# Kernel tuning notes

Measured on AMD Instinct MI355X. Metric: run time of the kernel, lower is better.

Reference implementation:

```python
import jax, jax.numpy as jnp
import numpy as np

B, N, CIN, H, W = 4, 1024, 256, 256, 256
R, C = 32, 32            # N = R*C table grid cells
PH, PW, SR = 3, 3, 2     # pool_size, sampling_ratio
D = 512                  # out_channels
SCALE = 0.25             # spatial_scale: image coords -> feature coords
IMG = 1024.0             # image size (H/SCALE)


def setup_inputs() -> dict:
    key = jax.random.key(0)
    ks = jax.random.split(key, 12)
    feats = jax.random.normal(ks[0], (B, CIN, H, W), jnp.float32)
    # build valid quadrilateral boxes (axis-aligned rectangles as 8-pt polys)
    x1 = jax.random.uniform(ks[1], (B, N), minval=0.0, maxval=IMG - 130.0)
    y1 = jax.random.uniform(ks[2], (B, N), minval=0.0, maxval=IMG - 130.0)
    bw = jax.random.uniform(ks[3], (B, N), minval=16.0, maxval=128.0)
    bh = jax.random.uniform(ks[4], (B, N), minval=16.0, maxval=128.0)
    x2, y2 = x1 + bw, y1 + bh
    boxes = jnp.stack([x1, y1, x2, y1, x2, y2, x1, y2], axis=-1)  # [B,N,8]
    img_sizes = jnp.full((B, 2), IMG, jnp.float32)
    IN = CIN * PH * PW
    W1 = jax.random.normal(ks[5], (IN, D), jnp.float32) * 0.02
    b1 = jnp.zeros((D,), jnp.float32)
    W2 = jax.random.normal(ks[6], (D, D), jnp.float32) * 0.02
    b2 = jnp.zeros((D,), jnp.float32)
    Wb = jax.random.normal(ks[7], (4, D), jnp.float32) * 0.02
    bb = jnp.zeros((D,), jnp.float32)
    g1 = jnp.ones((D,), jnp.float32); be1 = jnp.zeros((D,), jnp.float32)
    g2 = jnp.ones((D,), jnp.float32); be2 = jnp.zeros((D,), jnp.float32)
    return {"feats": feats, "boxes": boxes, "img_sizes": img_sizes,
            "W1": W1, "b1": b1, "W2": W2, "b2": b2, "Wb": Wb, "bb": bb,
            "g1": g1, "be1": be1, "g2": g2, "be2": be2}


def _layer_norm(x, g, b, eps=1e-5):
    mu = jnp.mean(x, axis=-1, keepdims=True)
    var = jnp.mean(jnp.square(x - mu), axis=-1, keepdims=True)
    return (x - mu) * jax.lax.rsqrt(var + eps) * g + b


def _bilinear(img, ys, xs):
    # img [Cin,H,W]; ys,xs [P] -> [Cin,P]; torchvision roi_align semantics:
    # zero outside (-1, dim); clamp into [0, dim-1] before interpolation.
    h, w = img.shape[1], img.shape[2]
    valid = (ys > -1.0) & (ys < h) & (xs > -1.0) & (xs < w)
    y = jnp.clip(ys, 0.0, h - 1.0)
    x = jnp.clip(xs, 0.0, w - 1.0)
    y0 = jnp.floor(y).astype(jnp.int32); x0 = jnp.floor(x).astype(jnp.int32)
    y1 = jnp.minimum(y0 + 1, h - 1);     x1 = jnp.minimum(x0 + 1, w - 1)
    ly = y - y0; lx = x - x0; hy = 1.0 - ly; hx = 1.0 - lx
    v = (img[:, y0, x0] * (hy * hx) + img[:, y0, x1] * (hy * lx)
         + img[:, y1, x0] * (ly * hx) + img[:, y1, x1] * (ly * lx))
    return v * valid


def _roi_align_one(img, bb):
    # img [Cin,H,W]; bb [N,4] already in feature coords -> [N,Cin,PH,PW]
    x1, y1, x2, y2 = bb[:, 0], bb[:, 1], bb[:, 2], bb[:, 3]
    rw = jnp.maximum(x2 - x1, 1.0); rh = jnp.maximum(y2 - y1, 1.0)
    binw = rw / PW; binh = rh / PH
    off = (jnp.arange(SR, dtype=jnp.float32) + 0.5) / SR
    gy = (jnp.arange(PH, dtype=jnp.float32)[:, None] + off[None, :]).reshape(-1)  # [PH*SR]
    gx = (jnp.arange(PW, dtype=jnp.float32)[:, None] + off[None, :]).reshape(-1)  # [PW*SR]
    ys = y1[:, None] + gy[None, :] * binh[:, None]  # [N,PH*SR]
    xs = x1[:, None] + gx[None, :] * binw[:, None]  # [N,PW*SR]
    YY = jnp.broadcast_to(ys[:, :, None], (bb.shape[0], PH * SR, PW * SR)).reshape(-1)
    XX = jnp.broadcast_to(xs[:, None, :], (bb.shape[0], PH * SR, PW * SR)).reshape(-1)
    vals = _bilinear(img, YY, XX)  # [Cin, N*PH*SR*PW*SR]
    vals = vals.reshape(CIN, bb.shape[0], PH, SR, PW, SR).mean(axis=(3, 5))
    return vals.transpose(1, 0, 2, 3)


def reference(feats, boxes, img_sizes, W1, b1, W2, b2, Wb, bb, g1, be1, g2, be2):
    # poly2bbox: [B,N,8] -> [B,N,4] axis-aligned boxes
    px, py = boxes[..., 0::2], boxes[..., 1::2]
    bbox = jnp.stack([px.min(-1), py.min(-1), px.max(-1), py.max(-1)], axis=-1)
    # rotated/regular RoIAlign (here bbox path), vmapped over batch images
    pooled = jax.vmap(_roi_align_one)(feats, bbox * SCALE)     # [B,N,Cin,PH,PW]
    flat = pooled.reshape(B, N, CIN * PH * PW)
    lines_feat = jax.nn.relu(flat @ W1 + b1) @ W2 + b2          # [B,N,D]
    # bbox positional embedding (coords normalized by image size)
    denom = jnp.concatenate([img_sizes, img_sizes], axis=-1)[:, None, :]  # [B,1,4] (w,h,w,h)
    pos = _layer_norm(bbox / denom @ Wb + bb, g1, be1)
    out = _layer_norm(lines_feat + pos, g2, be2)                # [B,N,D]
    # align_cells_feat: pack cells into grid [B,D,R,C] (uniform grid -> no pad)
    aligned = out.transpose(0, 2, 1).reshape(B, D, R, C)
    masks = jnp.ones((B, R, C), jnp.float32)
    return aligned, masks
```

## Files before the change

### kernel.cpp

```cpp
#include <hip/hip_runtime.h>
#include <hip/hip_bf16.h>
#include <cstdint>
#include <cstddef>

#define B_    4
#define N_    1024
#define CIN_  256
#define HW_   256
#define D_    512
#define INK_  2304
#define BN_   4096

typedef __attribute__((ext_vector_type(8))) short bf16x8;
typedef __attribute__((ext_vector_type(4))) float f32x4;
typedef __attribute__((ext_vector_type(4))) unsigned short us4;

#define AS1(p) ((const __attribute__((address_space(1))) void*)(p))
#define AS3(p) ((__attribute__((address_space(3))) void*)(p))

__device__ __forceinline__ unsigned short f2bf(float f) {
    union { float f; unsigned u; } v; v.f = f;
    unsigned r = v.u + 0x7fffu + ((v.u >> 16) & 1u);
    return (unsigned short)(r >> 16);
}

template <typename OutT>
__global__ __launch_bounds__(256) void k_t64(
    const float* __restrict__ src, OutT* __restrict__ dst,
    int Mrows, int Ncols, size_t sBatch, size_t dBatch)
{
    constexpr int PAD = (sizeof(OutT) == 2) ? 66 : 67;
    __shared__ OutT tile[64][PAD];
    const int n0 = blockIdx.x * 64;
    const int m0 = blockIdx.y * 64;
    const float* s = src + (size_t)blockIdx.z * sBatch;
    OutT* d = dst + (size_t)blockIdx.z * dBatch;
    const int t  = threadIdx.x;
    const int rr = t >> 4;
    const int cc = t & 15;

    #pragma unroll
    for (int i = 0; i < 4; ++i) {
        int row = i * 16 + rr;
        float4 v = *(const float4*)(s + (size_t)(m0 + row) * Ncols + n0 + cc * 4);
        if constexpr (sizeof(OutT) == 2) {
            tile[row][cc * 4 + 0] = f2bf(v.x);
            tile[row][cc * 4 + 1] = f2bf(v.y);
            tile[row][cc * 4 + 2] = f2bf(v.z);
            tile[row][cc * 4 + 3] = f2bf(v.w);
        } else {
            tile[row][cc * 4 + 0] = v.x;
            tile[row][cc * 4 + 1] = v.y;
            tile[row][cc * 4 + 2] = v.z;
            tile[row][cc * 4 + 3] = v.w;
        }
    }
    __syncthreads();
    #pragma unroll
    for (int i = 0; i < 4; ++i) {
        int p = i * 16 + rr;
        OutT v0 = tile[cc * 4 + 0][p];
        OutT v1 = tile[cc * 4 + 1][p];
        OutT v2 = tile[cc * 4 + 2][p];
        OutT v3 = tile[cc * 4 + 3][p];
        OutT* dp = d + (size_t)(n0 + p) * Mrows + m0 + cc * 4;
        if constexpr (sizeof(OutT) == 2) {
            *(us4*)dp = (us4){(unsigned short)v0, (unsigned short)v1,
                              (unsigned short)v2, (unsigned short)v3};
        } else {
            *(float4*)dp = make_float4(v0, v1, v2, v3);
        }
    }
}

__global__ __launch_bounds__(256) void k_roi3(
    const unsigned short* __restrict__ featsT, const float* __restrict__ boxes,
    unsigned short* __restrict__ flat)
{
    __shared__ int   so[4][36][4];
    __shared__ float sw[4][36][4];
    const int t = threadIdx.x;

    if (t < 144) {
        const int mbx = t / 36, s = t - mbx * 36;
        const int mbn = blockIdx.x * 4 + mbx;
        const float* bx = boxes + (size_t)mbn * 8;
        float xmn = fminf(fminf(bx[0], bx[2]), fminf(bx[4], bx[6]));
        float xmx = fmaxf(fmaxf(bx[0], bx[2]), fmaxf(bx[4], bx[6]));
        float ymn = fminf(fminf(bx[1], bx[3]), fminf(bx[5], bx[7]));
        float ymx = fmaxf(fmaxf(bx[1], bx[3]), fmaxf(bx[5], bx[7]));
        float sx1 = xmn * 0.25f, sy1 = ymn * 0.25f;
        float sx2 = xmx * 0.25f, sy2 = ymx * 0.25f;
        float rw = fmaxf(sx2 - sx1, 1.0f), rh = fmaxf(sy2 - sy1, 1.0f);
        float binw = rw * (1.0f / 3.0f), binh = rh * (1.0f / 3.0f);
        int row = s / 6, col = s % 6;
        float y = sy1 + (row * 0.5f + 0.25f) * binh;
        float x = sx1 + (col * 0.5f + 0.25f) * binw;
        float valid = (y > -1.0f && y < 256.0f && x > -1.0f && x < 256.0f) ? 1.0f : 0.0f;
        y = fminf(fmaxf(y, 0.0f), 255.0f);
        x = fminf(fmaxf(x, 0.0f), 255.0f);
        int y0 = (int)floorf(y), x0 = (int)floorf(x);
        int y1 = min(y0 + 1, 255), x1 = min(x0 + 1, 255);
        float ly = y - (float)y0, lx = x - (float)x0;
        float hy = 1.0f - ly, hx = 1.0f - lx;
        float m = 0.25f * valid;
        so[mbx][s][0] = y0 * HW_ + x0;  so[mbx][s][1] = y0 * HW_ + x1;
        so[mbx][s][2] = y1 * HW_ + x0;  so[mbx][s][3] = y1 * HW_ + x1;
        sw[mbx][s][0] = hy * hx * m;    sw[mbx][s][1] = hy * lx * m;
        sw[mbx][s][2] = ly * hx * m;    sw[mbx][s][3] = ly * lx * m;
    }
    __syncthreads();

    const int bxi = t >> 6;
    const int tid = t & 63;
    const int bn  = blockIdx.x * 4 + bxi;
    const int b   = bn >> 10;
    const uint2* basep = (const uint2*)featsT + (size_t)b * (65536ull * 64ull) + tid;

    float a0[9] = {0,0,0,0,0,0,0,0,0};
    float a1[9] = {0,0,0,0,0,0,0,0,0};
    float a2[9] = {0,0,0,0,0,0,0,0,0};
    float a3[9] = {0,0,0,0,0,0,0,0,0};
    #pragma unroll
    for (int j = 0; j < 36; ++j) {
        const int bin = ((j / 6) >> 1) * 3 + ((j % 6) >> 1);
        #pragma unroll
        for (int p = 0; p < 4; ++p) {
            float wgt = sw[bxi][j][p];
            uint2 u = basep[(size_t)so[bxi][j][p] << 6];
            a0[bin] += wgt * __uint_as_float(u.x << 16);
            a1[bin] += wgt * __uint_as_float(u.x & 0xffff0000u);
            a2[bin] += wgt * __uint_as_float(u.y << 16);
            a3[bin] += wgt * __uint_as_float(u.y & 0xffff0000u);
        }
    }

    unsigned short tmp[36];
    #pragma unroll
    for (int k = 0; k < 9; ++k) {
        tmp[k] = f2bf(a0[k]); tmp[9 + k] = f2bf(a1[k]);
        tmp[18 + k] = f2bf(a2[k]); tmp[27 + k] = f2bf(a3[k]);
    }
    unsigned* dst = (unsigned*)(flat + (size_t)bn * INK_ + tid * 36);
    #pragma unroll
    for (int k = 0; k < 18; ++k)
        dst[k] = (unsigned)tmp[2 * k] | ((unsigned)tmp[2 * k + 1] << 16);
}

template <int K, bool RELU_BF16OUT>
__global__ __launch_bounds__(256) void k_gemmB(
    const unsigned short* __restrict__ A,
    const unsigned short* __restrict__ Bt,
    const float* __restrict__ bias,
    unsigned short* __restrict__ Cbf,
    float* __restrict__ Cf)
{
    __shared__ __align__(16) unsigned short As[2][128 * 32];
    __shared__ __align__(16) unsigned short Bs[2][64 * 32];

    const int t = threadIdx.x;
    const int w = t >> 6;
    const int lane = t & 63;
    const int lane16 = lane & 15;
    const int q = lane >> 4;
    const int m0 = blockIdx.x * 128;
    const int n0 = blockIdx.y * 64;

    const int r4 = lane >> 2, c4 = lane & 3;
    const int c4s = c4 ^ (r4 >> 2);
    const unsigned short* gA0 = A + (size_t)(m0 + w * 16 + r4) * K + c4s * 8;
    const unsigned short* gA1 = gA0 + (size_t)64 * K;
    const unsigned short* gB  = Bt + (size_t)(n0 + w * 16 + r4) * K + c4s * 8;

    const int qs = q ^ ((lane16 >> 2) & 3);

    f32x4 acc[2][4] = {};

    __builtin_amdgcn_global_load_lds(AS1(gA0), AS3(&As[0][(w * 16) * 32]), 16, 0, 0);
    __builtin_amdgcn_global_load_lds(AS1(gA1), AS3(&As[0][(64 + w * 16) * 32]), 16, 0, 0);
    __builtin_amdgcn_global_load_lds(AS1(gB ), AS3(&Bs[0][(w * 16) * 32]), 16, 0, 0);
    gA0 += 32; gA1 += 32; gB += 32;

    int cur = 0;
    for (int k0 = 0; k0 < K; k0 += 32) {
        __syncthreads();
        if (k0 + 32 < K) {
            __builtin_amdgcn_global_load_lds(AS1(gA0), AS3(&As[cur ^ 1][(w * 16) * 32]), 16, 0, 0);
            __builtin_amdgcn_global_load_lds(AS1(gA1), AS3(&As[cur ^ 1][(64 + w * 16) * 32]), 16, 0, 0);
            __builtin_amdgcn_global_load_lds(AS1(gB ), AS3(&Bs[cur ^ 1][(w * 16) * 32]), 16, 0, 0);
            gA0 += 32; gA1 += 32; gB += 32;
        }
        bf16x8 a0 = *(const bf16x8*)&As[cur][(w * 32 + lane16) * 32 + qs * 8];
        bf16x8 a1 = *(const bf16x8*)&As[cur][(w * 32 + 16 + lane16) * 32 + qs * 8];
        #pragma unroll
        for (int nt = 0; nt < 4; ++nt) {
            bf16x8 bv = *(const bf16x8*)&Bs[cur][(nt * 16 + lane16) * 32 + qs * 8];
            acc[0][nt] = __builtin_amdgcn_mfma_f32_16x16x32_bf16(a0, bv, acc[0][nt], 0, 0, 0);
            acc[1][nt] = __builtin_amdgcn_mfma_f32_16x16x32_bf16(a1, bv, acc[1][nt], 0, 0, 0);
        }
        cur ^= 1;
    }

    #pragma unroll
    for (int nt = 0; nt < 4; ++nt) {
        int col = n0 + nt * 16 + lane16;
        float bs = bias[col];
        #pragma unroll
        for (int mg = 0; mg < 2; ++mg) {
            #pragma unroll
            for (int r = 0; r < 4; ++r) {
                int row = m0 + w * 32 + mg * 16 + q * 4 + r;
                float v = acc[mg][nt][r] + bs;
                if constexpr (RELU_BF16OUT) {
                    v = fmaxf(v, 0.0f);
                    Cbf[(size_t)row * D_ + col] = f2bf(v);
                } else {
                    Cf[(size_t)row * D_ + col] = v;
                }
            }
        }
    }
}

__global__ __launch_bounds__(256) void k_fuse2(
    const unsigned short* __restrict__ act,
    const unsigned short* __restrict__ W2t,
    const float* __restrict__ b2,
    const float* __restrict__ boxes,
    const float* __restrict__ img_sizes,
    const float* __restrict__ Wb,  const float* __restrict__ bbv,
    const float* __restrict__ g1,  const float* __restrict__ be1,
    const float* __restrict__ g2,  const float* __restrict__ be2,
    float* __restrict__ out)
{
    __shared__ __align__(16) unsigned short Bs[2][512 * 32];
    float* S2 = (float*)&Bs[0][0];

    const int t = threadIdx.x;
    const int w = t >> 6, l = t & 63;
    const int lane16 = l & 15, q = l >> 4;
    const int m0 = blockIdx.x * 16;
    const int b  = m0 >> 10;

    const unsigned short* gB = W2t + (size_t)(t >> 2) * D_
                             + (size_t)(((t & 3) ^ ((t >> 4) & 3)) * 8);
    #pragma unroll
    for (int i = 0; i < 8; ++i)
        __builtin_amdgcn_global_load_lds(AS1(gB + (size_t)i * 64 * D_),
            AS3(&Bs[0][(t >> 2) * 32 + (t & 3) * 8 + i * 2048]), 16, 0, 0);

    const int qs = q ^ ((lane16 >> 2) & 3);

    f32x4 acc[8] = {};
    const unsigned short* gA = act + (size_t)(m0 + lane16) * D_ + q * 8;

    int cur = 0;
    for (int k0 = 0; k0 < D_; k0 += 32) {
        __syncthreads();
        bf16x8 av = *(const bf16x8*)(gA + k0);
        if (k0 + 32 < D_) {
            #pragma unroll
            for (int i = 0; i < 8; ++i)
                __builtin_amdgcn_global_load_lds(AS1(gB + k0 + 32 + (size_t)i * 64 * D_),
                    AS3(&Bs[cur ^ 1][(t >> 2) * 32 + (t & 3) * 8 + i * 2048]), 16, 0, 0);
        }
        #pragma unroll
        for (int nt = 0; nt < 8; ++nt) {
            bf16x8 bv = *(const bf16x8*)&Bs[cur][(w * 128 + nt * 16 + lane16) * 32 + qs * 8];
            acc[nt] = __builtin_amdgcn_mfma_f32_16x16x32_bf16(av, bv, acc[nt], 0, 0, 0);
        }
        cur ^= 1;
    }
    __syncthreads();

    #pragma unroll
    for (int nt = 0; nt < 8; ++nt) {
        int col = w * 128 + nt * 16 + lane16;
        float bs = b2[col];
        #pragma unroll
        for (int r = 0; r < 4; ++r)
            S2[(q * 4 + r) * D_ + col] = acc[nt][r] + bs;
    }
    __syncthreads();

    const float si0 = img_sizes[b * 2], si1 = img_sizes[b * 2 + 1];
    #pragma unroll 1
    for (int j = 0; j < 4; ++j) {
        const int rho = w * 4 + j;
        const float* bx = boxes + (size_t)(m0 + rho) * 8;
        float xmn = fminf(fminf(bx[0], bx[2]), fminf(bx[4], bx[6]));
        float xmx = fmaxf(fmaxf(bx[0], bx[2]), fmaxf(bx[4], bx[6]));
        float ymn = fminf(fminf(bx[1], bx[3]), fminf(bx[5], bx[7]));
        float ymx = fmaxf(fmaxf(bx[1], bx[3]), fmaxf(bx[5], bx[7]));
        float q0 = xmn / si0, q1 = ymn / si1, q2 = xmx / si0, q3 = ymx / si1;

        float tp[8], su = 0.f, sq = 0.f;
        #pragma unroll
        for (int i = 0; i < 8; ++i) {
            int d = i * 64 + l;
            float v = q0 * Wb[d] + q1 * Wb[512 + d] + q2 * Wb[1024 + d]
                    + q3 * Wb[1536 + d] + bbv[d];
            tp[i] = v; su += v; sq += v * v;
        }
        #pragma unroll
        for (int off = 32; off > 0; off >>= 1) {
            su += __shfl_xor(su, off); sq += __shfl_xor(sq, off);
        }
        float mu = su * (1.0f / 512.0f);
        float rs = rsqrtf(sq * (1.0f / 512.0f) - mu * mu + 1e-5f);

        float sv[8]; su = 0.f; sq = 0.f;
        #pragma unroll
        for (int i = 0; i < 8; ++i) {
            int d = i * 64 + l;
            float p = (tp[i] - mu) * rs * g1[d] + be1[d];
            float s = S2[rho * D_ + d] + p;
            sv[i] = s; su += s; sq += s * s;
        }
        #pragma unroll
        for (int off = 32; off > 0; off >>= 1) {
            su += __shfl_xor(su, off); sq += __shfl_xor(sq, off);
        }
        float mu2 = su * (1.0f / 512.0f);
        float rs2 = rsqrtf(sq * (1.0f / 512.0f) - mu2 * mu2 + 1e-5f);

        #pragma unroll
        for (int i = 0; i < 8; ++i) {
            int d = i * 64 + l;
            S2[rho * D_ + d] = (sv[i] - mu2) * rs2 * g2[d] + be2[d];
        }
    }
    __syncthreads();

    const int nb = m0 & 1023;
    float* ob = out + (size_t)b * (D_ * N_) + nb;
    const int dd = t >> 2, part = t & 3;
    #pragma unroll
    for (int i = 0; i < 8; ++i) {
        int d = i * 64 + dd;
        float4 v;
        v.x = S2[(part * 4 + 0) * D_ + d];
        v.y = S2[(part * 4 + 1) * D_ + d];
        v.z = S2[(part * 4 + 2) * D_ + d];
        v.w = S2[(part * 4 + 3) * D_ + d];
        *(float4*)(ob + (size_t)d * N_ + part * 4) = v;
    }
    if (t < 16) out[(size_t)B_ * D_ * N_ + m0 + t] = 1.0f;
}

__global__ __launch_bounds__(256) void k_convert(
    const float* __restrict__ W1, const float* __restrict__ W2,
    unsigned short* __restrict__ W1t, unsigned short* __restrict__ W2t)
{
    int i = blockIdx.x * 256 + threadIdx.x;
    const int n1 = INK_ * D_;
    if (i < n1) {
        int n = i / INK_, k = i % INK_;
        W1t[i] = f2bf(W1[(size_t)k * D_ + n]);
    } else {
        int j = i - n1;
        if (j < D_ * D_) {
            int n = j / D_, k = j % D_;
            W2t[j] = f2bf(W2[(size_t)k * D_ + n]);
        }
    }
}

__global__ __launch_bounds__(256) void k_roi(
    const float* __restrict__ feats, const float* __restrict__ boxes,
    unsigned short* __restrict__ flat)
{
    __shared__ int   so[36][4];
    __shared__ float sw[36][4];
    const int bn = blockIdx.x;
    const int b  = bn >> 10;
    const int t  = threadIdx.x;

    if (t < 36) {
        const float* bx = boxes + (size_t)bn * 8;
        float xmn = fminf(fminf(bx[0], bx[2]), fminf(bx[4], bx[6]));
        float xmx = fmaxf(fmaxf(bx[0], bx[2]), fmaxf(bx[4], bx[6]));
        float ymn = fminf(fminf(bx[1], bx[3]), fminf(bx[5], bx[7]));
        float ymx = fmaxf(fmaxf(bx[1], bx[3]), fmaxf(bx[5], bx[7]));
        float sx1 = xmn * 0.25f, sy1 = ymn * 0.25f;
        float sx2 = xmx * 0.25f, sy2 = ymx * 0.25f;
        float rw = fmaxf(sx2 - sx1, 1.0f), rh = fmaxf(sy2 - sy1, 1.0f);
        float binw = rw * (1.0f / 3.0f), binh = rh * (1.0f / 3.0f);
        int row = t / 6, col = t % 6;
        float y = sy1 + (row * 0.5f + 0.25f) * binh;
        float x = sx1 + (col * 0.5f + 0.25f) * binw;
        float valid = (y > -1.0f && y < 256.0f && x > -1.0f && x < 256.0f) ? 1.0f : 0.0f;
        y = fminf(fmaxf(y, 0.0f), 255.0f);
        x = fminf(fmaxf(x, 0.0f), 255.0f);
        int y0 = (int)floorf(y), x0 = (int)floorf(x);
        int y1 = min(y0 + 1, 255), x1 = min(x0 + 1, 255);
        float ly = y - (float)y0, lx = x - (float)x0;
        float hy = 1.0f - ly, hx = 1.0f - lx;
        float m = 0.25f * valid;
        so[t][0] = y0 * HW_ + x0;  so[t][1] = y0 * HW_ + x1;
        so[t][2] = y1 * HW_ + x0;  so[t][3] = y1 * HW_ + x1;
        sw[t][0] = hy * hx * m;    sw[t][1] = hy * lx * m;
        sw[t][2] = ly * hx * m;    sw[t][3] = ly * lx * m;
    }
    __syncthreads();

    const float* base = feats + ((size_t)(b * CIN_ + t) << 16);
    float acc[9] = {0.f,0.f,0.f,0.f,0.f,0.f,0.f,0.f,0.f};
    #pragma unroll
    for (int j = 0; j < 36; ++j) {
        const int bin = ((j / 6) >> 1) * 3 + ((j % 6) >> 1);
        float v = sw[j][0] * base[so[j][0]] + sw[j][1] * base[so[j][1]]
                + sw[j][2] * base[so[j][2]] + sw[j][3] * base[so[j][3]];
        acc[bin] += v;
    }
    unsigned short* dst = flat + (size_t)bn * INK_ + t * 9;
    #pragma unroll
    for (int k = 0; k < 9; ++k) dst[k] = f2bf(acc[k]);
}

template <int K, bool RELU_BF16OUT>
__global__ __launch_bounds__(256) void k_gemm(
    const unsigned short* __restrict__ A,
    const unsigned short* __restrict__ Bt,
    const float* __restrict__ bias,
    unsigned short* __restrict__ Cbf,
    float* __restrict__ Cf)
{
    __shared__ __align__(16) unsigned short Asl[64 * 40];
    __shared__ __align__(16) unsigned short Bsl[64 * 40];

    const int t  = threadIdx.x;
    const int m0 = blockIdx.x * 64;
    const int n0 = blockIdx.y * 64;
    const int w  = t >> 6;
    const int l  = t & 63;
    const int lane16 = l & 15;
    const int q  = l >> 4;

    f32x4 acc[4] = {};

    const int srow = t >> 2;
    const int sch  = t & 3;
    const unsigned short* ga = A  + (size_t)(m0 + srow) * K + sch * 8;
    const unsigned short* gb = Bt + (size_t)(n0 + srow) * K + sch * 8;
    unsigned short* la = &Asl[srow * 40 + sch * 8];
    unsigned short* lb = &Bsl[srow * 40 + sch * 8];

    for (int k0 = 0; k0 < K; k0 += 32) {
        __syncthreads();
        *(bf16x8*)la = *(const bf16x8*)(ga + k0);
        *(bf16x8*)lb = *(const bf16x8*)(gb + k0);
        __syncthreads();
        bf16x8 af = *(const bf16x8*)&Asl[(w * 16 + lane16) * 40 + q * 8];
        #pragma unroll
        for (int nt = 0; nt < 4; ++nt) {
            bf16x8 bfv = *(const bf16x8*)&Bsl[(nt * 16 + lane16) * 40 + q * 8];
            acc[nt] = __builtin_amdgcn_mfma_f32_16x16x32_bf16(af, bfv, acc[nt], 0, 0, 0);
        }
    }

    #pragma unroll
    for (int nt = 0; nt < 4; ++nt) {
        int col = n0 + nt * 16 + lane16;
        float bs = bias[col];
        #pragma unroll
        for (int r = 0; r < 4; ++r) {
            int rowg = m0 + w * 16 + q * 4 + r;
            float v = acc[nt][r] + bs;
            if constexpr (RELU_BF16OUT) {
                v = fmaxf(v, 0.0f);
                Cbf[(size_t)rowg * D_ + col] = f2bf(v);
            } else {
                Cf[(size_t)rowg * D_ + col] = v;
            }
        }
    }
}

__device__ __forceinline__ void breduce2(float& a, float& b, float* red, int t) {
    #pragma unroll
    for (int off = 32; off > 0; off >>= 1) {
        a += __shfl_down(a, off);
        b += __shfl_down(b, off);
    }
    int w = t >> 6;
    if ((t & 63) == 0) { red[w] = a; red[4 + w] = b; }
    __syncthreads();
    a = red[0] + red[1] + red[2] + red[3];
    b = red[4] + red[5] + red[6] + red[7];
    __syncthreads();
}

__global__ __launch_bounds__(256) void k_tail(
    const float* __restrict__ lines, const float* __restrict__ boxes,
    const float* __restrict__ img_sizes,
    const float* __restrict__ Wb,  const float* __restrict__ bbv,
    const float* __restrict__ g1,  const float* __restrict__ be1,
    const float* __restrict__ g2,  const float* __restrict__ be2,
    float* __restrict__ out)
{
    __shared__ float red[8];
    const int row = blockIdx.x;
    const int b = row >> 10, n = row & 1023;
    const int t = threadIdx.x;

    const float* bx = boxes + (size_t)row * 8;
    float xmn = fminf(fminf(bx[0], bx[2]), fminf(bx[4], bx[6]));
    float xmx = fmaxf(fmaxf(bx[0], bx[2]), fmaxf(bx[4], bx[6]));
    float ymn = fminf(fminf(bx[1], bx[3]), fminf(bx[5], bx[7]));
    float ymx = fmaxf(fmaxf(bx[1], bx[3]), fmaxf(bx[5], bx[7]));
    float s0 = img_sizes[b * 2], s1 = img_sizes[b * 2 + 1];
    float q0 = xmn / s0, q1 = ymn / s1, q2 = xmx / s0, q3 = ymx / s1;

    float tv[2], sv[2];
    float sum = 0.f, sumsq = 0.f;
    #pragma unroll
    for (int i = 0; i < 2; ++i) {
        int d = t + i * 256;
        float v = q0 * Wb[d] + q1 * Wb[512 + d] + q2 * Wb[1024 + d] + q3 * Wb[1536 + d] + bbv[d];
        tv[i] = v; sum += v; sumsq += v * v;
    }
    breduce2(sum, sumsq, red, t);
    float mu = sum * (1.0f / 512.0f);
    float var = sumsq * (1.0f / 512.0f) - mu * mu;
    float rs = rsqrtf(var + 1e-5f);

    sum = 0.f; sumsq = 0.f;
    #pragma unroll
    for (int i = 0; i < 2; ++i) {
        int d = t + i * 256;
        float p = (tv[i] - mu) * rs * g1[d] + be1[d];
        float s = lines[(size_t)row * D_ + d] + p;
        sv[i] = s; sum += s; sumsq += s * s;
    }
    breduce2(sum, sumsq, red, t);
    float mu2 = sum * (1.0f / 512.0f);
    float var2 = sumsq * (1.0f / 512.0f) - mu2 * mu2;
    float rs2 = rsqrtf(var2 + 1e-5f);

    #pragma unroll
    for (int i = 0; i < 2; ++i) {
        int d = t + i * 256;
        float o = (sv[i] - mu2) * rs2 * g2[d] + be2[d];
        out[(size_t)b * (D_ * N_) + (size_t)d * N_ + n] = o;
    }
}

__global__ __launch_bounds__(256) void k_mask(float* __restrict__ out) {
    int i = blockIdx.x * 256 + threadIdx.x;
    if (i < B_ * 32 * 32) out[(size_t)B_ * D_ * N_ + i] = 1.0f;
}

extern "C" void kernel_launch(void* const* d_in, const int* in_sizes, int n_in,
                              void* d_out, int out_size, void* d_ws, size_t ws_size,
                              hipStream_t stream)
{
    const float* feats = (const float*)d_in[0];
    const float* boxes = (const float*)d_in[1];
    const float* img   = (const float*)d_in[2];
    const float* W1    = (const float*)d_in[3];
    const float* b1    = (const float*)d_in[4];
    const float* W2    = (const float*)d_in[5];
    const float* b2    = (const float*)d_in[6];
    const float* Wb    = (const float*)d_in[7];
    const float* bbv   = (const float*)d_in[8];
    const float* g1    = (const float*)d_in[9];
    const float* be1   = (const float*)d_in[10];
    const float* g2    = (const float*)d_in[11];
    const float* be2   = (const float*)d_in[12];
    float* out = (float*)d_out;
    char* ws = (char*)d_ws;

    const size_t OFF_FEATST = 0;
    const size_t OFF_W1T    = 134217728;
    const size_t OFF_W2T    = 136577024;
    const size_t OFF_FLAT   = 137101312;
    const size_t OFF_ACT    = 155975680;
    const size_t NEED       = 160169984;

    if (ws_size >= NEED) {
        unsigned short* featsT = (unsigned short*)(ws + OFF_FEATST);
        unsigned short* W1t    = (unsigned short*)(ws + OFF_W1T);
        unsigned short* W2t    = (unsigned short*)(ws + OFF_W2T);
        unsigned short* flat   = (unsigned short*)(ws + OFF_FLAT);
        unsigned short* act    = (unsigned short*)(ws + OFF_ACT);

        k_t64<unsigned short><<<dim3(HW_*HW_/64, CIN_/64, B_), 256, 0, stream>>>(
            feats, featsT, CIN_, HW_*HW_, (size_t)CIN_*HW_*HW_, (size_t)CIN_*HW_*HW_);
        k_t64<unsigned short><<<dim3(D_/64, INK_/64, 1), 256, 0, stream>>>(
            W1, W1t, INK_, D_, 0, 0);
        k_t64<unsigned short><<<dim3(D_/64, D_/64, 1), 256, 0, stream>>>(
            W2, W2t, D_, D_, 0, 0);

        k_roi3<<<BN_/4, 256, 0, stream>>>(featsT, boxes, flat);

        dim3 gg(32, 8);
        k_gemmB<INK_, true><<<gg, 256, 0, stream>>>(flat, W1t, b1, act, nullptr);

        k_fuse2<<<BN_/16, 256, 0, stream>>>(act, W2t, b2, boxes, img,
                                            Wb, bbv, g1, be1, g2, be2, out);
    } else {
        unsigned short* W1t  = (unsigned short*)(ws);
        unsigned short* W2t  = (unsigned short*)(ws + 2359296);
        unsigned short* flat = (unsigned short*)(ws + 2883584);
        unsigned short* act  = (unsigned short*)(ws + 21757952);
        float*          lines= (float*)(ws + 25952256);

        const int convTotal = INK_ * D_ + D_ * D_;
        k_convert<<<(convTotal + 255) / 256, 256, 0, stream>>>(W1, W2, W1t, W2t);
        k_roi<<<BN_, 256, 0, stream>>>(feats, boxes, flat);
        dim3 gg(64, 8);
        k_gemm<INK_, true ><<<gg, 256, 0, stream>>>(flat, W1t, b1, act, nullptr);
        k_gemm<D_,   false><<<gg, 256, 0, stream>>>(act,  W2t, b2, nullptr, lines);
        k_tail<<<BN_, 256, 0, stream>>>(lines, boxes, img, Wb, bbv, g1, be1, g2, be2, out);
        k_mask<<<16, 256, 0, stream>>>(out);
    }
}
```

Baseline: 505.1 us.

## Shrink first GEMM tile to 64x64 and read W2 directly from global in fuse kernel

The first GEMM's M tile is halved from 128 to 64 rows, doubling the grid from 256 to 512 blocks so more of the CUs are busy, at the cost of less reuse of each loaded W1 tile. The fused second GEMM no longer stages W2 through double-buffered LDS with barriers. Each wave now loads its W2 fragments straight from global memory, relying on the cache, and LDS use drops to the output staging buffer. This removes the barrier and LDS traffic but exposes global-load latency to the MFMA loop.

```diff
diff --git a/kernel.cpp b/kernel.cpp
--- a/kernel.cpp
+++ b/kernel.cpp
@@ -148,14 +148,14 @@
 }
 
 template <int K, bool RELU_BF16OUT>
-__global__ __launch_bounds__(256) void k_gemmB(
+__global__ __launch_bounds__(256) void k_gemmB64(
     const unsigned short* __restrict__ A,
     const unsigned short* __restrict__ Bt,
     const float* __restrict__ bias,
     unsigned short* __restrict__ Cbf,
     float* __restrict__ Cf)
 {
-    __shared__ __align__(16) unsigned short As[2][128 * 32];
+    __shared__ __align__(16) unsigned short As[2][64 * 32];
     __shared__ __align__(16) unsigned short Bs[2][64 * 32];
 
     const int t = threadIdx.x;
@@ -163,40 +163,36 @@
     const int lane = t & 63;
     const int lane16 = lane & 15;
     const int q = lane >> 4;
-    const int m0 = blockIdx.x * 128;
+    const int m0 = blockIdx.x * 64;
     const int n0 = blockIdx.y * 64;
 
-    const int r4 = lane >> 2, c4 = lane & 3;
-    const int c4s = c4 ^ (r4 >> 2);
-    const unsigned short* gA0 = A + (size_t)(m0 + w * 16 + r4) * K + c4s * 8;
-    const unsigned short* gA1 = gA0 + (size_t)64 * K;
-    const unsigned short* gB  = Bt + (size_t)(n0 + w * 16 + r4) * K + c4s * 8;
+    const int srow = t >> 2;
+    const int c4s  = (t & 3) ^ ((t >> 4) & 3);
+    const unsigned short* gA = A  + (size_t)(m0 + srow) * K + c4s * 8;
+    const unsigned short* gB = Bt + (size_t)(n0 + srow) * K + c4s * 8;
+    const int ldst = srow * 32 + (t & 3) * 8;
 
     const int qs = q ^ ((lane16 >> 2) & 3);
 
-    f32x4 acc[2][4] = {};
-
-    __builtin_amdgcn_global_load_lds(AS1(gA0), AS3(&As[0][(w * 16) * 32]), 16, 0, 0);
-    __builtin_amdgcn_global_load_lds(AS1(gA1), AS3(&As[0][(64 + w * 16) * 32]), 16, 0, 0);
-    __builtin_amdgcn_global_load_lds(AS1(gB ), AS3(&Bs[0][(w * 16) * 32]), 16, 0, 0);
-    gA0 += 32; gA1 += 32; gB += 32;
+    f32x4 acc[4] = {};
+
+    __builtin_amdgcn_global_load_lds(AS1(gA), AS3(&As[0][ldst & ~1023] + (ldst & 1023)), 16, 0, 0);
+    __builtin_amdgcn_global_load_lds(AS1(gB), AS3(&Bs[0][0] + ldst), 16, 0, 0);
+    gA += 32; gB += 32;
 
     int cur = 0;
     for (int k0 = 0; k0 < K; k0 += 32) {
         __syncthreads();
         if (k0 + 32 < K) {
-            __builtin_amdgcn_global_load_lds(AS1(gA0), AS3(&As[cur ^ 1][(w * 16) * 32]), 16, 0, 0);
-            __builtin_amdgcn_global_load_lds(AS1(gA1), AS3(&As[cur ^ 1][(64 + w * 16) * 32]), 16, 0, 0);
-            __builtin_amdgcn_global_load_lds(AS1(gB ), AS3(&Bs[cur ^ 1][(w * 16) * 32]), 16, 0, 0);
-            gA0 += 32; gA1 += 32; gB += 32;
-        }
-        bf16x8 a0 = *(const bf16x8*)&As[cur][(w * 32 + lane16) * 32 + qs * 8];
-        bf16x8 a1 = *(const bf16x8*)&As[cur][(w * 32 + 16 + lane16) * 32 + qs * 8];
+            __builtin_amdgcn_global_load_lds(AS1(gA), AS3(&As[cur ^ 1][0] + ldst), 16, 0, 0);
+            __builtin_amdgcn_global_load_lds(AS1(gB), AS3(&Bs[cur ^ 1][0] + ldst), 16, 0, 0);
+            gA += 32; gB += 32;
+        }
+        bf16x8 av = *(const bf16x8*)&As[cur][(w * 16 + lane16) * 32 + qs * 8];
         #pragma unroll
         for (int nt = 0; nt < 4; ++nt) {
             bf16x8 bv = *(const bf16x8*)&Bs[cur][(nt * 16 + lane16) * 32 + qs * 8];
-            acc[0][nt] = __builtin_amdgcn_mfma_f32_16x16x32_bf16(a0, bv, acc[0][nt], 0, 0, 0);
-            acc[1][nt] = __builtin_amdgcn_mfma_f32_16x16x32_bf16(a1, bv, acc[1][nt], 0, 0, 0);
+            acc[nt] = __builtin_amdgcn_mfma_f32_16x16x32_bf16(av, bv, acc[nt], 0, 0, 0);
         }
         cur ^= 1;
     }
@@ -206,17 +202,14 @@
         int col = n0 + nt * 16 + lane16;
         float bs = bias[col];
         #pragma unroll
-        for (int mg = 0; mg < 2; ++mg) {
-            #pragma unroll
-            for (int r = 0; r < 4; ++r) {
-                int row = m0 + w * 32 + mg * 16 + q * 4 + r;
-                float v = acc[mg][nt][r] + bs;
-                if constexpr (RELU_BF16OUT) {
-                    v = fmaxf(v, 0.0f);
-                    Cbf[(size_t)row * D_ + col] = f2bf(v);
-                } else {
-                    Cf[(size_t)row * D_ + col] = v;
-                }
+        for (int r = 0; r < 4; ++r) {
+            int row = m0 + w * 16 + q * 4 + r;
+            float v = acc[nt][r] + bs;
+            if constexpr (RELU_BF16OUT) {
+                v = fmaxf(v, 0.0f);
+                Cbf[(size_t)row * D_ + col] = f2bf(v);
+            } else {
+                Cf[(size_t)row * D_ + col] = v;
             }
         }
     }
@@ -233,8 +226,7 @@
     const float* __restrict__ g2,  const float* __restrict__ be2,
     float* __restrict__ out)
 {
-    __shared__ __align__(16) unsigned short Bs[2][512 * 32];
-    float* S2 = (float*)&Bs[0][0];
+    __shared__ float S2[16 * D_];
 
     const int t = threadIdx.x;
     const int w = t >> 6, l = t & 63;
@@ -242,36 +234,19 @@
     const int m0 = blockIdx.x * 16;
     const int b  = m0 >> 10;
 
-    const unsigned short* gB = W2t + (size_t)(t >> 2) * D_
-                             + (size_t)(((t & 3) ^ ((t >> 4) & 3)) * 8);
-    #pragma unroll
-    for (int i = 0; i < 8; ++i)
-        __builtin_amdgcn_global_load_lds(AS1(gB + (size_t)i * 64 * D_),
-            AS3(&Bs[0][(t >> 2) * 32 + (t & 3) * 8 + i * 2048]), 16, 0, 0);
-
-    const int qs = q ^ ((lane16 >> 2) & 3);
-
     f32x4 acc[8] = {};
     const unsigned short* gA = act + (size_t)(m0 + lane16) * D_ + q * 8;
-
-    int cur = 0;
+    const unsigned short* gW = W2t + (size_t)(w * 128 + lane16) * D_ + q * 8;
+
+    #pragma unroll 2
     for (int k0 = 0; k0 < D_; k0 += 32) {
-        __syncthreads();
         bf16x8 av = *(const bf16x8*)(gA + k0);
-        if (k0 + 32 < D_) {
-            #pragma unroll
-            for (int i = 0; i < 8; ++i)
-                __builtin_amdgcn_global_load_lds(AS1(gB + k0 + 32 + (size_t)i * 64 * D_),
-                    AS3(&Bs[cur ^ 1][(t >> 2) * 32 + (t & 3) * 8 + i * 2048]), 16, 0, 0);
-        }
         #pragma unroll
         for (int nt = 0; nt < 8; ++nt) {
-            bf16x8 bv = *(const bf16x8*)&Bs[cur][(w * 128 + nt * 16 + lane16) * 32 + qs * 8];
+            bf16x8 bv = *(const bf16x8*)(gW + (size_t)(nt * 16) * D_ + k0);
             acc[nt] = __builtin_amdgcn_mfma_f32_16x16x32_bf16(av, bv, acc[nt], 0, 0, 0);
         }
-        cur ^= 1;
-    }
-    __syncthreads();
+    }
 
     #pragma unroll
     for (int nt = 0; nt < 8; ++nt) {
@@ -594,8 +569,8 @@
 
         k_roi3<<<BN_/4, 256, 0, stream>>>(featsT, boxes, flat);
 
-        dim3 gg(32, 8);
-        k_gemmB<INK_, true><<<gg, 256, 0, stream>>>(flat, W1t, b1, act, nullptr);
+        dim3 gg(64, 8);
+        k_gemmB64<INK_, true><<<gg, 256, 0, stream>>>(flat, W1t, b1, act, nullptr);
 
         k_fuse2<<<BN_/16, 256, 0, stream>>>(act, W2t, b2, boxes, img,
                                             Wb, bbv, g1, be1, g2, be2, out);
```

New measurement: 514.6 us. About the same (+1.9%).
